# Performance work log

Hardware: AMD Instinct MI355X
Metric: run time of the kernel (lower is better)

## Reference

```python
import jax, jax.numpy as jnp
import numpy as np

B, IN_DIM, HID, ODE_STEPS = 8192, 1024, 1024, 6
DT = 1.0


def setup_inputs() -> dict:
    key = jax.random.key(0)
    ks = jax.random.split(key, 8)
    s = 0.02  # init scale for stability
    return {
        "x": jax.random.normal(ks[0], (B, IN_DIM), dtype=jnp.float32),
        "h": jax.random.normal(ks[1], (B, HID), dtype=jnp.float32),
        "log_tau": jnp.zeros((HID,), dtype=jnp.float32),
        "W_in_w": jax.random.normal(ks[2], (HID, IN_DIM), dtype=jnp.float32) * s,
        "W_in_b": jnp.zeros((HID,), dtype=jnp.float32),
        "W_rec_w": jax.random.normal(ks[3], (HID, HID), dtype=jnp.float32) * s,
        "W_gate_w": jax.random.normal(ks[4], (HID, IN_DIM + HID), dtype=jnp.float32) * s,
        "W_gate_b": jnp.zeros((HID,), dtype=jnp.float32),
    }


def reference(x, h, log_tau, W_in_w, W_in_b, W_rec_w, W_gate_w, W_gate_b):
    # torch Linear: y = x @ W.T + b, W:(out,in)
    tau = jnp.exp(log_tau)                      # (HID,)
    input_drive = x @ W_in_w.T + W_in_b         # (B,HID), loop-invariant
    # W_gate acts on concat([x, h]); split into x-block and h-block.
    Wg_x = W_gate_w[:, :IN_DIM]
    Wg_h = W_gate_w[:, IN_DIM:]
    gate_x = x @ Wg_x.T + W_gate_b              # (B,HID), loop-invariant
    sub_dt = DT / ODE_STEPS
    scale = sub_dt / tau                        # (HID,)

    def step(h, _):
        gate = jax.nn.sigmoid(gate_x + h @ Wg_h.T)
        f = -h + gate * jnp.tanh(input_drive + h @ W_rec_w.T)
        return h + scale * f, None

    h, _ = jax.lax.scan(step, h, None, length=ODE_STEPS)
    return (h, h)
```

## Files before the change

### kernel.cpp

```cpp
#include <hip/hip_runtime.h>
#include <hip/hip_bf16.h>
#include <stdint.h>

#define B_DIM 8192
#define IN_DIMC 1024
#define HIDC 1024
#define K_DIM 1024
#define ODE_STEPS 6

typedef float f32x4 __attribute__((ext_vector_type(4)));
typedef short bf16x8 __attribute__((ext_vector_type(8)));

__device__ __forceinline__ float bf2f(unsigned short u) {
    union { unsigned int u; float f; } c; c.u = ((unsigned int)u) << 16; return c.f;
}
__device__ __forceinline__ unsigned short f2bf(float f) {
    union { float f; unsigned int u; } c; c.f = f;
    unsigned int u = c.u;
    return (unsigned short)((u + 0x7fffu + ((u >> 16) & 1u)) >> 16);
}
__device__ __forceinline__ float fast_tanh(float x) {
    float e = __expf(2.0f * x);
    return 1.0f - 2.0f / (e + 1.0f);
}

constexpr size_t XN    = (size_t)B_DIM * IN_DIMC;
constexpr size_t HN    = (size_t)B_DIM * HIDC;
constexpr size_t WINN  = (size_t)HIDC * IN_DIMC;
constexpr size_t WRECN = (size_t)HIDC * HIDC;
constexpr size_t WGN   = (size_t)HIDC * (IN_DIMC + HIDC);
constexpr size_t TOTQ  = (XN + HN + WINN + WRECN + WGN) / 4;

__global__ __launch_bounds__(256) void convert_all(
    const float* __restrict__ x, const float* __restrict__ h,
    const float* __restrict__ win, const float* __restrict__ wrec,
    const float* __restrict__ wgate,
    unsigned short* __restrict__ x_bf, unsigned short* __restrict__ h_bf,
    unsigned short* __restrict__ win_bf, unsigned short* __restrict__ wrec_bf,
    unsigned short* __restrict__ wgx_bf, unsigned short* __restrict__ wgh_bf)
{
    size_t q = (size_t)blockIdx.x * 256 + threadIdx.x;
    if (q >= TOTQ) return;
    size_t e = q * 4;
    const float* src; unsigned short* dst; size_t si, di;
    if (e < XN)                          { src = x;    si = e;                       dst = x_bf;    di = si; }
    else if (e < XN + HN)                { src = h;    si = e - XN;                  dst = h_bf;    di = si; }
    else if (e < XN + HN + WINN)         { src = win;  si = e - XN - HN;             dst = win_bf;  di = si; }
    else if (e < XN + HN + WINN + WRECN) { src = wrec; si = e - XN - HN - WINN;      dst = wrec_bf; di = si; }
    else {
        size_t i = e - XN - HN - WINN - WRECN;
        size_t row = i >> 11, col = i & 2047;
        src = wgate; si = i;
        if (col < 1024) { dst = wgx_bf; di = row * 1024 + col; }
        else            { dst = wgh_bf; di = row * 1024 + (col - 1024); }
    }
    float4 v = *(const float4*)(src + si);
    ushort4 o;
    o.x = f2bf(v.x); o.y = f2bf(v.y); o.z = f2bf(v.z); o.w = f2bf(v.w);
    *(ushort4*)(dst + di) = o;
}

constexpr int BM = 128, BN = 64, BK = 32;
constexpr int NT = HIDC / BN;

__device__ __forceinline__ void gload_lds16(const void* g, void* l) {
    __builtin_amdgcn_global_load_lds(
        (const __attribute__((address_space(1))) void*)g,
        (__attribute__((address_space(3))) void*)l, 16, 0, 0);
}

template<bool STEP>
__global__ __launch_bounds__(256, 3) void ltc_gemm(
    const unsigned short* __restrict__ A,
    const unsigned short* __restrict__ B1,
    const unsigned short* __restrict__ B2,
    const unsigned short* __restrict__ GX, const unsigned short* __restrict__ ID,
    const float* __restrict__ h_in, const float* __restrict__ log_tau,
    float* __restrict__ h_out, float* __restrict__ h_out2,
    unsigned short* __restrict__ hbf_out,
    const float* __restrict__ bias1, const float* __restrict__ bias2,
    unsigned short* __restrict__ GX_out, unsigned short* __restrict__ ID_out)
{
    __shared__ __attribute__((aligned(16))) unsigned short lA[BM * BK];
    __shared__ __attribute__((aligned(16))) unsigned short lB1[BN * BK];
    __shared__ __attribute__((aligned(16))) unsigned short lB2[BN * BK];

    const int tid = threadIdx.x;
    const int w = tid >> 6, l = tid & 63;
    const int mt = blockIdx.x / NT, nt = blockIdx.x % NT;
    const int m0 = mt * BM, n0 = nt * BN;
    const int wm = (w >> 1) * 64, wn = (w & 1) * 32;
    const int lrow = l >> 2, lcol = (l & 3) * 8;
    const int lm = l & 15, lq = l >> 4;

    f32x4 acc1[4][2], acc2[4][2];
    f32x4 z4 = {0.f, 0.f, 0.f, 0.f};
    #pragma unroll
    for (int i = 0; i < 4; i++)
        #pragma unroll
        for (int j = 0; j < 2; j++) { acc1[i][j] = z4; acc2[i][j] = z4; }

    const int arow = w * 32;
    const unsigned short* Bsrc = (w < 2) ? B1 : B2;
    unsigned short* lBdst = (w < 2) ? lB1 : lB2;
    const int brow = (w & 1) * 32;

    for (int k0 = 0; k0 < K_DIM; k0 += BK) {
        #pragma unroll
        for (int i = 0; i < 2; i++) {
            int ra = arow + i * 16;
            int rb = brow + i * 16;
            gload_lds16(A    + (size_t)(m0 + ra + lrow) * K_DIM + k0 + lcol, &lA[ra * BK]);
            gload_lds16(Bsrc + (size_t)(n0 + rb + lrow) * K_DIM + k0 + lcol, &lBdst[rb * BK]);
        }
        __syncthreads();

        bf16x8 af[4], f1[2], f2[2];
        #pragma unroll
        for (int mi = 0; mi < 4; mi++)
            af[mi] = *(const bf16x8*)&lA[(wm + mi * 16 + lm) * BK + lq * 8];
        #pragma unroll
        for (int ni = 0; ni < 2; ni++) {
            f1[ni] = *(const bf16x8*)&lB1[(wn + ni * 16 + lm) * BK + lq * 8];
            f2[ni] = *(const bf16x8*)&lB2[(wn + ni * 16 + lm) * BK + lq * 8];
        }
        #pragma unroll
        for (int mi = 0; mi < 4; mi++)
            #pragma unroll
            for (int ni = 0; ni < 2; ni++) {
                acc1[mi][ni] = __builtin_amdgcn_mfma_f32_16x16x32_bf16(af[mi], f1[ni], acc1[mi][ni], 0, 0, 0);
                acc2[mi][ni] = __builtin_amdgcn_mfma_f32_16x16x32_bf16(af[mi], f2[ni], acc2[mi][ni], 0, 0, 0);
            }
        __syncthreads();
    }

    constexpr float subdt = 1.0f / (float)ODE_STEPS;
    #pragma unroll
    for (int mi = 0; mi < 4; mi++) {
        #pragma unroll
        for (int ni = 0; ni < 2; ni++) {
            const int gmb = m0 + wm + mi * 16 + lq * 4;
            const int gn  = n0 + wn + ni * 16 + lm;
            if (STEP) {
                const float sc = subdt * __expf(-log_tau[gn]);
                #pragma unroll
                for (int r = 0; r < 4; r++) {
                    size_t idx = (size_t)(gmb + r) * HIDC + gn;
                    float gx = bf2f(GX[idx]) + acc1[mi][ni][r];
                    float dr = bf2f(ID[idx]) + acc2[mi][ni][r];
                    float g  = 1.0f / (1.0f + __expf(-gx));
                    float t  = fast_tanh(dr);
                    float hv = h_in[idx];
                    float hn = fmaf(sc, g * t - hv, hv);
                    h_out[idx] = hn;
                    hbf_out[idx] = f2bf(hn);
                    if (h_out2) h_out2[idx] = hn;
                }
            } else {
                const float b1 = bias1[gn], b2 = bias2[gn];
                #pragma unroll
                for (int r = 0; r < 4; r++) {
                    size_t idx = (size_t)(gmb + r) * HIDC + gn;
                    GX_out[idx] = f2bf(acc1[mi][ni][r] + b1);
                    ID_out[idx] = f2bf(acc2[mi][ni][r] + b2);
                }
            }
        }
    }
}

extern "C" void kernel_launch(void* const* d_in, const int* in_sizes, int n_in,
                              void* d_out, int out_size, void* d_ws, size_t ws_size,
                              hipStream_t stream)
{
    const float* x    = (const float*)d_in[0];
    const float* h    = (const float*)d_in[1];
    const float* ltau = (const float*)d_in[2];
    const float* winw = (const float*)d_in[3];
    const float* winb = (const float*)d_in[4];
    const float* wrec = (const float*)d_in[5];
    const float* wg   = (const float*)d_in[6];
    const float* wgb  = (const float*)d_in[7];

    char* ws = (char*)d_ws;
    unsigned short* x_bf    = (unsigned short*)ws; ws += XN * 2;
    unsigned short* h_bf0   = (unsigned short*)ws; ws += HN * 2;
    unsigned short* h_bf1   = (unsigned short*)ws; ws += HN * 2;
    unsigned short* win_bf  = (unsigned short*)ws; ws += WINN * 2;
    unsigned short* wrec_bf = (unsigned short*)ws; ws += WRECN * 2;
    unsigned short* wgx_bf  = (unsigned short*)ws; ws += WINN * 2;
    unsigned short* wgh_bf  = (unsigned short*)ws; ws += WRECN * 2;
    unsigned short* GXb     = (unsigned short*)ws; ws += HN * 2;
    unsigned short* IDb     = (unsigned short*)ws; ws += HN * 2;

    float* hout  = (float*)d_out;
    float* hout2 = hout + (size_t)B_DIM * HIDC;

    convert_all<<<(int)(TOTQ / 256), 256, 0, stream>>>(
        x, h, winw, wrec, wg, x_bf, h_bf0, win_bf, wrec_bf, wgx_bf, wgh_bf);

    const int grid = (B_DIM / BM) * NT;
    ltc_gemm<false><<<grid, 256, 0, stream>>>(
        x_bf, wgx_bf, win_bf,
        nullptr, nullptr, nullptr, nullptr, nullptr, nullptr, nullptr,
        wgb, winb, GXb, IDb);

    unsigned short* hbf[2] = {h_bf0, h_bf1};
    for (int s = 0; s < ODE_STEPS; s++) {
        const float* hin = (s == 0) ? h : (const float*)hout;
        float* o2 = (s == ODE_STEPS - 1) ? hout2 : nullptr;
        ltc_gemm<true><<<grid, 256, 0, stream>>>(
            hbf[s & 1], wgh_bf, wrec_bf,
            GXb, IDb, hin, ltau, hout, o2, hbf[(s + 1) & 1],
            nullptr, nullptr, nullptr, nullptr);
    }
}
```

Before: 555.2 us.

## Switch GEMM to 32x32x16 MFMA with BK=64 and XOR-swizzled LDS layout

Raises the K tile from 32 to 64, swaps the 16x16x32 MFMA for the 32x32x16 variant so each fragment load feeds more math, and XOR-swizzles the LDS columns to avoid bank conflicts on the fragment reads. The aim is fewer barriers per K and more MFMA work per LDS read. The cost is double the LDS per block, which may reduce occupancy under the 3-blocks launch bound, and a new epilogue mapping that has to match the 32x32 output layout.

Measured after the change: 608.4 us. 1.1x slower.

```diff
diff --git a/kernel.cpp b/kernel.cpp
--- a/kernel.cpp
+++ b/kernel.cpp
@@ -9,6 +9,7 @@
 #define ODE_STEPS 6
 
 typedef float f32x4 __attribute__((ext_vector_type(4)));
+typedef float f32x16 __attribute__((ext_vector_type(16)));
 typedef short bf16x8 __attribute__((ext_vector_type(8)));
 
 __device__ __forceinline__ float bf2f(unsigned short u) {
@@ -60,7 +61,7 @@
     *(ushort4*)(dst + di) = o;
 }
 
-constexpr int BM = 128, BN = 64, BK = 32;
+constexpr int BM = 128, BN = 64, BK = 64;
 constexpr int NT = HIDC / BN;
 
 __device__ __forceinline__ void gload_lds16(const void* g, void* l) {
@@ -90,79 +91,78 @@
     const int mt = blockIdx.x / NT, nt = blockIdx.x % NT;
     const int m0 = mt * BM, n0 = nt * BN;
     const int wm = (w >> 1) * 64, wn = (w & 1) * 32;
-    const int lrow = l >> 2, lcol = (l & 3) * 8;
-    const int lm = l & 15, lq = l >> 4;
-
-    f32x4 acc1[4][2], acc2[4][2];
-    f32x4 z4 = {0.f, 0.f, 0.f, 0.f};
+
+    const int srow8 = l >> 3;
+    const int scol  = ((l & 7) ^ srow8) * 8;
+
+    const int lr = l & 31, lh = l >> 5;
+    const int rsw = lr & 7;
+
+    f32x16 acc1[2], acc2[2];
     #pragma unroll
-    for (int i = 0; i < 4; i++)
-        #pragma unroll
-        for (int j = 0; j < 2; j++) { acc1[i][j] = z4; acc2[i][j] = z4; }
-
-    const int arow = w * 32;
-    const unsigned short* Bsrc = (w < 2) ? B1 : B2;
-    unsigned short* lBdst = (w < 2) ? lB1 : lB2;
-    const int brow = (w & 1) * 32;
+    for (int i = 0; i < 2; i++) {
+        acc1[i] = (f32x16)0.0f;
+        acc2[i] = (f32x16)0.0f;
+    }
 
     for (int k0 = 0; k0 < K_DIM; k0 += BK) {
         #pragma unroll
+        for (int i = 0; i < 4; i++) {
+            int R = w * 32 + i * 8;
+            gload_lds16(A + (size_t)(m0 + R + srow8) * K_DIM + k0 + scol, &lA[R * BK]);
+        }
+        #pragma unroll
         for (int i = 0; i < 2; i++) {
-            int ra = arow + i * 16;
-            int rb = brow + i * 16;
-            gload_lds16(A    + (size_t)(m0 + ra + lrow) * K_DIM + k0 + lcol, &lA[ra * BK]);
-            gload_lds16(Bsrc + (size_t)(n0 + rb + lrow) * K_DIM + k0 + lcol, &lBdst[rb * BK]);
+            int R = w * 16 + i * 8;
+            gload_lds16(B1 + (size_t)(n0 + R + srow8) * K_DIM + k0 + scol, &lB1[R * BK]);
+            gload_lds16(B2 + (size_t)(n0 + R + srow8) * K_DIM + k0 + scol, &lB2[R * BK]);
         }
         __syncthreads();
 
-        bf16x8 af[4], f1[2], f2[2];
-        #pragma unroll
-        for (int mi = 0; mi < 4; mi++)
-            af[mi] = *(const bf16x8*)&lA[(wm + mi * 16 + lm) * BK + lq * 8];
-        #pragma unroll
-        for (int ni = 0; ni < 2; ni++) {
-            f1[ni] = *(const bf16x8*)&lB1[(wn + ni * 16 + lm) * BK + lq * 8];
-            f2[ni] = *(const bf16x8*)&lB2[(wn + ni * 16 + lm) * BK + lq * 8];
-        }
-        #pragma unroll
-        for (int mi = 0; mi < 4; mi++)
+        #pragma unroll
+        for (int kc = 0; kc < 4; kc++) {
+            const int csw = ((kc * 2 + lh) ^ rsw) * 8;
+            bf16x8 b1f = *(const bf16x8*)&lB1[(wn + lr) * BK + csw];
+            bf16x8 b2f = *(const bf16x8*)&lB2[(wn + lr) * BK + csw];
             #pragma unroll
-            for (int ni = 0; ni < 2; ni++) {
-                acc1[mi][ni] = __builtin_amdgcn_mfma_f32_16x16x32_bf16(af[mi], f1[ni], acc1[mi][ni], 0, 0, 0);
-                acc2[mi][ni] = __builtin_amdgcn_mfma_f32_16x16x32_bf16(af[mi], f2[ni], acc2[mi][ni], 0, 0, 0);
+            for (int mi = 0; mi < 2; mi++) {
+                bf16x8 af = *(const bf16x8*)&lA[(wm + mi * 32 + lr) * BK + csw];
+                acc1[mi] = __builtin_amdgcn_mfma_f32_32x32x16_bf16(af, b1f, acc1[mi], 0, 0, 0);
+                acc2[mi] = __builtin_amdgcn_mfma_f32_32x32x16_bf16(af, b2f, acc2[mi], 0, 0, 0);
             }
+        }
         __syncthreads();
     }
 
     constexpr float subdt = 1.0f / (float)ODE_STEPS;
+    const int gn = n0 + wn + lr;
+    float sc = 0.f, b1 = 0.f, b2 = 0.f;
+    if (STEP) sc = subdt * __expf(-log_tau[gn]);
+    else { b1 = bias1[gn]; b2 = bias2[gn]; }
+
     #pragma unroll
-    for (int mi = 0; mi < 4; mi++) {
-        #pragma unroll
-        for (int ni = 0; ni < 2; ni++) {
-            const int gmb = m0 + wm + mi * 16 + lq * 4;
-            const int gn  = n0 + wn + ni * 16 + lm;
-            if (STEP) {
-                const float sc = subdt * __expf(-log_tau[gn]);
-                #pragma unroll
-                for (int r = 0; r < 4; r++) {
-                    size_t idx = (size_t)(gmb + r) * HIDC + gn;
-                    float gx = bf2f(GX[idx]) + acc1[mi][ni][r];
-                    float dr = bf2f(ID[idx]) + acc2[mi][ni][r];
-                    float g  = 1.0f / (1.0f + __expf(-gx));
-                    float t  = fast_tanh(dr);
+    for (int mi = 0; mi < 2; mi++) {
+        const int rbase = m0 + wm + mi * 32 + 4 * lh;
+        #pragma unroll
+        for (int g = 0; g < 4; g++) {
+            #pragma unroll
+            for (int r = 0; r < 4; r++) {
+                const int grow = rbase + r + 8 * g;
+                const size_t idx = (size_t)grow * HIDC + gn;
+                const float v1 = acc1[mi][g * 4 + r];
+                const float v2 = acc2[mi][g * 4 + r];
+                if (STEP) {
+                    float gx = bf2f(GX[idx]) + v1;
+                    float dr = bf2f(ID[idx]) + v2;
+                    float gt = fast_tanh(dr) / (1.0f + __expf(-gx));
                     float hv = h_in[idx];
-                    float hn = fmaf(sc, g * t - hv, hv);
+                    float hn = fmaf(sc, gt - hv, hv);
                     h_out[idx] = hn;
                     hbf_out[idx] = f2bf(hn);
                     if (h_out2) h_out2[idx] = hn;
-                }
-            } else {
-                const float b1 = bias1[gn], b2 = bias2[gn];
-                #pragma unroll
-                for (int r = 0; r < 4; r++) {
-                    size_t idx = (size_t)(gmb + r) * HIDC + gn;
-                    GX_out[idx] = f2bf(acc1[mi][ni][r] + b1);
-                    ID_out[idx] = f2bf(acc2[mi][ni][r] + b2);
+                } else {
+                    GX_out[idx] = f2bf(v1 + b1);
+                    ID_out[idx] = f2bf(v2 + b2);
                 }
             }
         }
```

## Store GX/ID and fp32 state in fragment-native interleaved layout for vector I/O

Applied to the files above, without the earlier changes.

Packs the loop-invariant gate and input-drive terms into a single per-lane interleaved buffer, and keeps the fp32 hidden state in a fragment-native scratch buffer. Both can then be read and written with 16-byte vector accesses in the step epilogue instead of strided scalar accesses. It also skips the fp32 output writes on intermediate steps and the bf16 copy on the last step. The cost is an extra workspace buffer and a layout tied to the tile and wave mapping.

Result: faster. 521.1 us (-6.1%).

```diff
diff --git a/kernel.cpp b/kernel.cpp
--- a/kernel.cpp
+++ b/kernel.cpp
@@ -10,6 +10,7 @@
 
 typedef float f32x4 __attribute__((ext_vector_type(4)));
 typedef short bf16x8 __attribute__((ext_vector_type(8)));
+typedef unsigned short u16x8 __attribute__((ext_vector_type(8)));
 
 __device__ __forceinline__ float bf2f(unsigned short u) {
     union { unsigned int u; float f; } c; c.u = ((unsigned int)u) << 16; return c.f;
@@ -74,12 +75,15 @@
     const unsigned short* __restrict__ A,
     const unsigned short* __restrict__ B1,
     const unsigned short* __restrict__ B2,
-    const unsigned short* __restrict__ GX, const unsigned short* __restrict__ ID,
-    const float* __restrict__ h_in, const float* __restrict__ log_tau,
-    float* __restrict__ h_out, float* __restrict__ h_out2,
+    const unsigned short* __restrict__ GXID,
+    const float* __restrict__ h_init,
+    float* __restrict__ h_nat,
+    const float* __restrict__ log_tau,
+    float* __restrict__ h_out,
+    float* __restrict__ h_out2,
     unsigned short* __restrict__ hbf_out,
     const float* __restrict__ bias1, const float* __restrict__ bias2,
-    unsigned short* __restrict__ GX_out, unsigned short* __restrict__ ID_out)
+    unsigned short* __restrict__ GXID_out)
 {
     __shared__ __attribute__((aligned(16))) unsigned short lA[BM * BK];
     __shared__ __attribute__((aligned(16))) unsigned short lB1[BN * BK];
@@ -135,35 +139,56 @@
     }
 
     constexpr float subdt = 1.0f / (float)ODE_STEPS;
+    const size_t wslot = (((size_t)blockIdx.x * 4 + w) * 8) * 64 + l;
+
     #pragma unroll
     for (int mi = 0; mi < 4; mi++) {
         #pragma unroll
         for (int ni = 0; ni < 2; ni++) {
             const int gmb = m0 + wm + mi * 16 + lq * 4;
             const int gn  = n0 + wn + ni * 16 + lm;
+            const size_t slot = wslot + (size_t)(mi * 2 + ni) * 64;
             if (STEP) {
                 const float sc = subdt * __expf(-log_tau[gn]);
+                u16x8 gi = *(const u16x8*)&GXID[slot * 8];
+                f32x4 st;
+                if (h_init) {
+                    #pragma unroll
+                    for (int r = 0; r < 4; r++)
+                        st[r] = h_init[(size_t)(gmb + r) * HIDC + gn];
+                } else {
+                    st = *(const f32x4*)&h_nat[slot * 4];
+                }
+                f32x4 hn;
                 #pragma unroll
                 for (int r = 0; r < 4; r++) {
-                    size_t idx = (size_t)(gmb + r) * HIDC + gn;
-                    float gx = bf2f(GX[idx]) + acc1[mi][ni][r];
-                    float dr = bf2f(ID[idx]) + acc2[mi][ni][r];
-                    float g  = 1.0f / (1.0f + __expf(-gx));
-                    float t  = fast_tanh(dr);
-                    float hv = h_in[idx];
-                    float hn = fmaf(sc, g * t - hv, hv);
-                    h_out[idx] = hn;
-                    hbf_out[idx] = f2bf(hn);
-                    if (h_out2) h_out2[idx] = hn;
+                    float gx = bf2f((unsigned short)gi[r])     + acc1[mi][ni][r];
+                    float dr = bf2f((unsigned short)gi[4 + r]) + acc2[mi][ni][r];
+                    float gt = fast_tanh(dr) / (1.0f + __expf(-gx));
+                    hn[r] = fmaf(sc, gt - st[r], st[r]);
+                }
+                if (h_out) {
+                    #pragma unroll
+                    for (int r = 0; r < 4; r++) {
+                        size_t idx = (size_t)(gmb + r) * HIDC + gn;
+                        h_out[idx]  = hn[r];
+                        h_out2[idx] = hn[r];
+                    }
+                } else {
+                    *(f32x4*)&h_nat[slot * 4] = hn;
+                    #pragma unroll
+                    for (int r = 0; r < 4; r++)
+                        hbf_out[(size_t)(gmb + r) * HIDC + gn] = f2bf(hn[r]);
                 }
             } else {
                 const float b1 = bias1[gn], b2 = bias2[gn];
+                u16x8 o;
                 #pragma unroll
                 for (int r = 0; r < 4; r++) {
-                    size_t idx = (size_t)(gmb + r) * HIDC + gn;
-                    GX_out[idx] = f2bf(acc1[mi][ni][r] + b1);
-                    ID_out[idx] = f2bf(acc2[mi][ni][r] + b2);
-                }
+                    o[r]     = f2bf(acc1[mi][ni][r] + b1);
+                    o[4 + r] = f2bf(acc2[mi][ni][r] + b2);
+                }
+                *(u16x8*)&GXID_out[slot * 8] = o;
             }
         }
     }
@@ -190,8 +215,8 @@
     unsigned short* wrec_bf = (unsigned short*)ws; ws += WRECN * 2;
     unsigned short* wgx_bf  = (unsigned short*)ws; ws += WINN * 2;
     unsigned short* wgh_bf  = (unsigned short*)ws; ws += WRECN * 2;
-    unsigned short* GXb     = (unsigned short*)ws; ws += HN * 2;
-    unsigned short* IDb     = (unsigned short*)ws; ws += HN * 2;
+    unsigned short* GXID    = (unsigned short*)ws; ws += HN * 2 * 2;
+    float*          h_nat   = (float*)ws;          ws += HN * 4;
 
     float* hout  = (float*)d_out;
     float* hout2 = hout + (size_t)B_DIM * HIDC;
@@ -203,15 +228,18 @@
     ltc_gemm<false><<<grid, 256, 0, stream>>>(
         x_bf, wgx_bf, win_bf,
         nullptr, nullptr, nullptr, nullptr, nullptr, nullptr, nullptr,
-        wgb, winb, GXb, IDb);
+        wgb, winb, GXID);
 
     unsigned short* hbf[2] = {h_bf0, h_bf1};
     for (int s = 0; s < ODE_STEPS; s++) {
-        const float* hin = (s == 0) ? h : (const float*)hout;
-        float* o2 = (s == ODE_STEPS - 1) ? hout2 : nullptr;
+        const bool last = (s == ODE_STEPS - 1);
         ltc_gemm<true><<<grid, 256, 0, stream>>>(
             hbf[s & 1], wgh_bf, wrec_bf,
-            GXb, IDb, hin, ltau, hout, o2, hbf[(s + 1) & 1],
-            nullptr, nullptr, nullptr, nullptr);
-    }
-}
+            GXID,
+            (s == 0) ? h : nullptr,
+            h_nat, ltau,
+            last ? hout : nullptr, last ? hout2 : nullptr,
+            last ? nullptr : hbf[(s + 1) & 1],
+            nullptr, nullptr, nullptr);
+    }
+}
```
